# Performance work log

Measured on AMD Instinct MI355X. Metric: run time of the kernel, lower is better.

The kernel has to match this reference:

```python
import jax, jax.numpy as jnp
import numpy as np

E = 1024
H = 16
HD = 64
DI = E // 16  # 64, GRU hidden size
VOCAB = 32000
B, T = 2, 2048


def adaptive_pool_matrix(l_in, l_out):
    # PyTorch AdaptiveAvgPool1d: out[i] = mean(in[floor(i*l_in/l_out) : ceil((i+1)*l_in/l_out)])
    P = np.zeros((l_in, l_out), np.float32)
    for i in range(l_out):
        s = (i * l_in) // l_out
        e = -((-(i + 1) * l_in) // l_out)
        P[s:e, i] = 1.0 / (e - s)
    return jnp.asarray(P)


def gru(x, wih, whh):
    # x: [B, T, DI]; wih/whh: [3*DI, DI]; no bias; gate order (r, z, n)
    h_dim = whh.shape[1]
    xw = jnp.einsum('btd,gd->btg', x, wih)  # [B, T, 3*DI]

    def step(h, xw_t):
        hw = h @ whh.T
        r = jax.nn.sigmoid(xw_t[:, :h_dim] + hw[:, :h_dim])
        z = jax.nn.sigmoid(xw_t[:, h_dim:2 * h_dim] + hw[:, h_dim:2 * h_dim])
        n = jnp.tanh(xw_t[:, 2 * h_dim:] + r * hw[:, 2 * h_dim:])
        h_new = (1.0 - z) * n + z * h
        return h_new, h_new

    h0 = jnp.zeros((x.shape[0], h_dim), x.dtype)
    _, hs = jax.lax.scan(step, h0, jnp.swapaxes(xw, 0, 1))
    return jnp.swapaxes(hs, 0, 1)  # [B, T, DI]


def pos_embed(x, gru_wih, gru_whh, lin_w, p_pos, p_proj):
    # x: [B, T, E]. Pools act on the feature dim (torch last-dim after permute).
    x_proj = x @ p_proj            # [B, T, E-DI]
    pos = gru(x @ p_pos, gru_wih, gru_whh)  # [B, T, DI]
    out = jnp.concatenate([pos, x_proj], axis=-1) @ lin_w.T
    return out + x


def layernorm(x, w, b, eps=1e-5):
    mu = jnp.mean(x, axis=-1, keepdims=True)
    var = jnp.var(x, axis=-1, keepdims=True)
    return (x - mu) * jax.lax.rsqrt(var + eps) * w + b


def setup_inputs() -> dict:
    key = jax.random.key(0)
    ks = jax.random.split(key, 16)
    s = 0.02
    return {
        'x': jax.random.normal(ks[0], (B, T, E), jnp.float32),
        'token_ids': jax.random.randint(ks[1], (B, T), 0, VOCAB, jnp.int32),
        'q_gru_wih': jax.random.normal(ks[2], (3 * DI, DI), jnp.float32) * s,
        'q_gru_whh': jax.random.normal(ks[3], (3 * DI, DI), jnp.float32) * s,
        'q_lin_w': jax.random.normal(ks[4], (E, E), jnp.float32) * s,
        'k_gru_wih': jax.random.normal(ks[5], (3 * DI, DI), jnp.float32) * s,
        'k_gru_whh': jax.random.normal(ks[6], (3 * DI, DI), jnp.float32) * s,
        'k_lin_w': jax.random.normal(ks[7], (E, E), jnp.float32) * s,
        'v_emb': jax.random.normal(ks[8], (VOCAB, E), jnp.float32) * s + 1.0,
        'q_ln_w': jnp.ones((E,), jnp.float32),
        'q_ln_b': jnp.zeros((E,), jnp.float32),
        'k_ln_w': jnp.ones((E,), jnp.float32),
        'k_ln_b': jnp.zeros((E,), jnp.float32),
        'out_w': jax.random.normal(ks[9], (E, E), jnp.float32) * s,
        'out_b': jnp.zeros((E,), jnp.float32),
    }


def reference(x, token_ids, q_gru_wih, q_gru_whh, q_lin_w, k_gru_wih, k_gru_whh,
              k_lin_w, v_emb, q_ln_w, q_ln_b, k_ln_w, k_ln_b, out_w, out_b):
    p_pos = adaptive_pool_matrix(E, DI)
    p_proj = adaptive_pool_matrix(E, E - DI)

    q = pos_embed(x, q_gru_wih, q_gru_whh, q_lin_w, p_pos, p_proj)
    k = pos_embed(x, k_gru_wih, k_gru_whh, k_lin_w, p_pos, p_proj)
    v = jax.nn.silu(x) * v_emb[token_ids]  # [B, T, E]

    q = layernorm(q, q_ln_w, q_ln_b)
    k = layernorm(k, k_ln_w, k_ln_b)

    # [B, T, E] -> [B, H, T, HD]
    def split_heads(t):
        return t.reshape(B, T, H, HD).transpose(0, 2, 1, 3)

    qh, kh, vh = split_heads(q), split_heads(k), split_heads(v)

    scores = jnp.einsum('bhtd,bhsd->bhts', qh, kh) / jnp.sqrt(jnp.float32(HD))
    # Original code: attn_weights += attn_weights.masked_fill(mask, -inf)
    # => unmasked scores are DOUBLED; masked (future) positions become -inf.
    causal = jnp.triu(jnp.ones((T, T), bool), k=1)  # True above diagonal
    scores = jnp.where(causal, -jnp.inf, scores * 2.0)
    attn = jax.nn.softmax(scores, axis=-1)

    out = jnp.einsum('bhts,bhsd->bhtd', attn, vh)  # [B, H, T, HD]
    out = out.transpose(0, 2, 1, 3).reshape(B, T, E)
    return out @ out_w.T + out_b
```

## Files before the change

kernel.cpp:

```cpp
#include <hip/hip_runtime.h>


namespace {

constexpr int B_ = 2, T_ = 2048, E_ = 1024, H_ = 16, HD_ = 64, G3_ = 192, M_ = B_ * T_;
constexpr float SRg = -1.4426950408889634f;
constexpr float SNg = 2.8853900817779268f;

typedef _Float16 f16;
typedef _Float16 f16x8 __attribute__((ext_vector_type(8)));
typedef _Float16 f16x4 __attribute__((ext_vector_type(4)));
typedef _Float16 f16x2 __attribute__((ext_vector_type(2)));
typedef float f32x4 __attribute__((ext_vector_type(4)));

__device__ __forceinline__ f32x4 mfma16(f16x8 a, f16x8 b, f32x4 c) {
  return __builtin_amdgcn_mfma_f32_16x16x32_f16(a, b, c, 0, 0, 0);
}

#if __has_builtin(__builtin_amdgcn_fdot2)
__device__ __forceinline__ float fdot2(f16x2 a, f16x2 b, float c) {
  return __builtin_amdgcn_fdot2(a, b, c, false);
}
#else
__device__ __forceinline__ float fdot2(f16x2 a, f16x2 b, float c) {
  return c + (float)a[0] * (float)b[0] + (float)a[1] * (float)b[1];
}
#endif

__device__ __forceinline__ float exp2_(float x) {
#if __has_builtin(__builtin_amdgcn_exp2f)
  return __builtin_amdgcn_exp2f(x);
#else
  return exp2f(x);
#endif
}
__device__ __forceinline__ float rcp_(float x) {
#if __has_builtin(__builtin_amdgcn_rcpf)
  return __builtin_amdgcn_rcpf(x);
#else
  return 1.f / x;
#endif
}

__device__ __forceinline__ void stage_w_f32(const float* __restrict__ Wf,
                                            f16 (*Bs)[72], int n0, int kt,
                                            int tid) {
#pragma unroll
  for (int it = 0; it < 4; ++it) {
    const int r = it * 32 + (tid >> 3);
    const int cs = (tid & 7) * 8;
    const float* src = Wf + (size_t)(n0 + r) * E_ + kt + cs;
    float4 w0 = *(const float4*)src;
    float4 w1 = *(const float4*)(src + 4);
    f16x8 o = {(f16)w0.x, (f16)w0.y, (f16)w0.z, (f16)w0.w,
               (f16)w1.x, (f16)w1.y, (f16)w1.z, (f16)w1.w};
    *(f16x8*)&Bs[r][cs] = o;
  }
}

__global__ __launch_bounds__(256) void k_prep(
    const float* __restrict__ x, const int* __restrict__ tok,
    const float* __restrict__ wihq, const float* __restrict__ wihk,
    const float* __restrict__ v_emb,
    f16* __restrict__ vh, f16* __restrict__ aq, f16* __restrict__ ak,
    float* __restrict__ xwq, float* __restrict__ xwk) {
  __shared__ float xs[E_];
  __shared__ float xp[64];
  const int row = blockIdx.x;
  const int b = row >> 11, t = row & (T_ - 1);
  const int tid = threadIdx.x;
  const float* xrow = x + (size_t)row * E_;
  {
    const int tk = tok[row];
    float4 xv = ((const float4*)xrow)[tid];
    ((float4*)xs)[tid] = xv;
    float4 ev = ((const float4*)(v_emb + (size_t)tk * E_))[tid];
    f16x4 o;
    o[0] = (f16)(xv.x / (1.f + __expf(-xv.x)) * ev.x);
    o[1] = (f16)(xv.y / (1.f + __expf(-xv.y)) * ev.y);
    o[2] = (f16)(xv.z / (1.f + __expf(-xv.z)) * ev.z);
    o[3] = (f16)(xv.w / (1.f + __expf(-xv.w)) * ev.w);
    const int e0 = tid * 4;
    const size_t voff = ((size_t)(b * H_ + (e0 >> 6)) * T_ + t) * HD_ + (e0 & 63);
    *(f16x4*)(vh + voff) = o;
  }
  __syncthreads();
  if (tid < 64) {
    float s = 0.f;
#pragma unroll
    for (int j = 0; j < 16; ++j) s += xs[tid * 16 + j];
    xp[tid] = s * (1.f / 16.f);
  }
  for (int i = tid; i < 960; i += 256) {
    int s0 = (i * 1024) / 960;
    int e0 = ((i + 1) * 1024 + 959) / 960;
    float m = xs[s0];
    if (e0 - s0 == 2) m = (m + xs[s0 + 1]) * 0.5f;
    f16 hv = (f16)m;
    aq[(size_t)row * E_ + 64 + i] = hv;
    ak[(size_t)row * E_ + 64 + i] = hv;
  }
  __syncthreads();
  for (int o = tid; o < 2 * G3_; o += 256) {
    const int chain = o / G3_, g = o % G3_;
    const float* wrow = (chain ? wihk : wihq) + (size_t)g * 64;
    float acc = 0.f;
#pragma unroll
    for (int c = 0; c < 16; ++c) {
      float4 wv = *(const float4*)(wrow + c * 4);
      acc += xp[c * 4] * wv.x + xp[c * 4 + 1] * wv.y +
             xp[c * 4 + 2] * wv.z + xp[c * 4 + 3] * wv.w;
    }
    const float sc = (g < 128) ? SRg : SNg;
    (chain ? xwk : xwq)[(size_t)row * G3_ + g] = acc * sc;
  }
}

__device__ __forceinline__ void gru_core(const float* __restrict__ xw,
                                         const float* __restrict__ whh,
                                         f16* __restrict__ a, int lane) {
  __builtin_amdgcn_s_setprio(3);
  f16x2 wr[32], wz[32], wn[32];
#pragma unroll
  for (int i = 0; i < 32; ++i) {
    wr[i] = {(f16)(whh[(size_t)lane * 64 + i] * SRg),
             (f16)(whh[(size_t)lane * 64 + i + 32] * SRg)};
    wz[i] = {(f16)(whh[(size_t)(64 + lane) * 64 + i] * SRg),
             (f16)(whh[(size_t)(64 + lane) * 64 + i + 32] * SRg)};
    wn[i] = {(f16)(whh[(size_t)(128 + lane) * 64 + i] * SNg),
             (f16)(whh[(size_t)(128 + lane) * 64 + i + 32] * SNg)};
  }
  float h = 0.f;
  float xr = xw[lane], xz = xw[64 + lane], xn = xw[128 + lane];
  f16* ap = a + lane;
  for (int t = 0; t < T_; ++t) {
    const unsigned hu = (unsigned)__builtin_bit_cast(unsigned short, (f16)h);
    int va = (int)hu, vb = (int)hu;
    asm volatile("v_permlane32_swap_b32 %0, %1" : "+v"(va), "+v"(vb));
    const int pk = (int)(hu | ((unsigned)va << 16));
    const int tn = (t + 1 < T_) ? t + 1 : t;
    const float* nx = xw + (size_t)tn * G3_;
    const float nxr = nx[lane], nxz = nx[64 + lane], nxn = nx[128 + lane];
    float ar = xr, az = xz, an = 0.f;
#pragma unroll
    for (int i = 0; i < 32; ++i) {
      const f16x2 hh = __builtin_bit_cast(f16x2, __builtin_amdgcn_readlane(pk, i));
      ar = fdot2(wr[i], hh, ar);
      an = fdot2(wn[i], hh, an);
      az = fdot2(wz[i], hh, az);
    }
    const float r = rcp_(1.f + exp2_(ar));
    const float p2 = fmaf(r, an, xn);
    const float n = fmaf(-2.f, rcp_(1.f + exp2_(p2)), 1.f);
    const float z = rcp_(1.f + exp2_(az));
    h = fmaf(z, h - n, n);
    ap[(size_t)t * E_] = (f16)h;
    xr = nxr; xz = nxz; xn = nxn;
  }
}

__global__ __launch_bounds__(256, 1) void k_mega(
    const float* __restrict__ xwq, const float* __restrict__ xwk,
    const float* __restrict__ whhq, const float* __restrict__ whhk,
    f16* __restrict__ aq, f16* __restrict__ ak,
    const float* __restrict__ WQf, const float* __restrict__ WKf,
    const float* __restrict__ x,
    float* __restrict__ QPRE, float* __restrict__ KPRE,
    const float* __restrict__ out_w, f16* __restrict__ WO) {
  __shared__ __align__(16) f16 As[128][72];
  __shared__ __align__(16) f16 Bs[128][72];
  const int bx = blockIdx.x;
  const int tid = threadIdx.x;
  if (bx == 0) {
    const int wid = tid >> 6, lane = tid & 63;
    const int qk = wid >> 1, b = wid & 1;
    const float* xw = (qk ? xwk : xwq) + (size_t)b * T_ * G3_;
    const float* whh = qk ? whhk : whhq;
    f16* a = (qk ? ak : aq) + (size_t)b * T_ * E_;
    gru_core(xw, whh, a, lane);
    return;
  }
  if (bx <= 512) {
    const int bid = bx - 1;
    const int chain = bid >> 8, tile = bid & 255;
    const int m0 = (tile >> 3) * 128, n0 = (tile & 7) * 128;
    const f16* A = chain ? ak : aq;
    const float* Wf = chain ? WKf : WQf;
    float* C = chain ? KPRE : QPRE;
    const int wid = tid >> 6, lane = tid & 63;
    const int wr = wid >> 1, wc = wid & 1;
    const int lg = lane >> 4, lc = lane & 15;
    f32x4 acc[4][4] = {};
    for (int kt = 64; kt < E_; kt += 64) {
#pragma unroll
      for (int it = 0; it < 4; ++it) {
        const int r = it * 32 + (tid >> 3);
        const int cs = (tid & 7) * 8;
        *(f16x8*)&As[r][cs] = *(const f16x8*)(A + (size_t)(m0 + r) * E_ + kt + cs);
      }
      stage_w_f32(Wf, Bs, n0, kt, tid);
      __syncthreads();
      f16x8 af[4][2], bf[4][2];
#pragma unroll
      for (int mi = 0; mi < 4; ++mi)
#pragma unroll
        for (int ks = 0; ks < 2; ++ks) {
          af[mi][ks] = *(const f16x8*)&As[wr * 64 + mi * 16 + lc][ks * 32 + lg * 8];
          bf[mi][ks] = *(const f16x8*)&Bs[wc * 64 + mi * 16 + lc][ks * 32 + lg * 8];
        }
#pragma unroll
      for (int mi = 0; mi < 4; ++mi)
#pragma unroll
        for (int ni = 0; ni < 4; ++ni)
#pragma unroll
          for (int ks = 0; ks < 2; ++ks)
            acc[mi][ni] = mfma16(af[mi][ks], bf[ni][ks], acc[mi][ni]);
      __syncthreads();
    }
#pragma unroll
    for (int mi = 0; mi < 4; ++mi) {
      const int r0 = m0 + wr * 64 + mi * 16 + lg * 4;
#pragma unroll
      for (int ni = 0; ni < 4; ++ni) {
        const int col = n0 + wc * 64 + ni * 16 + lc;
#pragma unroll
        for (int q = 0; q < 4; ++q) {
          const size_t idx = (size_t)(r0 + q) * E_ + col;
          C[idx] = acc[mi][ni][q] + x[idx];
        }
      }
    }
    return;
  }
  {
    const int cb = bx - 513;
    for (int i = cb * 256 + tid; i < E_ * E_ / 4; i += 8 * 256) {
      float4 v = ((const float4*)out_w)[i];
      f16x4 o = {(f16)v.x, (f16)v.y, (f16)v.z, (f16)v.w};
      *(f16x4*)(WO + (size_t)i * 4) = o;
    }
  }
}

__global__ __launch_bounds__(256) void k_fix(
    const f16* __restrict__ aq, const f16* __restrict__ ak,
    const float* __restrict__ WQf, const float* __restrict__ WKf,
    float* __restrict__ QPRE, float* __restrict__ KPRE) {
  __shared__ __align__(16) f16 As[128][72];
  __shared__ __align__(16) f16 Bs[128][72];
  const int chain = blockIdx.z;
  const f16* A = chain ? ak : aq;
  const float* Wf = chain ? WKf : WQf;
  float* C = chain ? KPRE : QPRE;
  const int m0 = blockIdx.x * 128, n0 = blockIdx.y * 128;
  const int tid = threadIdx.x;
  const int wid = tid >> 6, lane = tid & 63;
  const int wr = wid >> 1, wc = wid & 1;
  const int lg = lane >> 4, lc = lane & 15;
#pragma unroll
  for (int it = 0; it < 4; ++it) {
    const int r = it * 32 + (tid >> 3);
    const int cs = (tid & 7) * 8;
    *(f16x8*)&As[r][cs] = *(const f16x8*)(A + (size_t)(m0 + r) * E_ + cs);
  }
  stage_w_f32(Wf, Bs, n0, 0, tid);
  __syncthreads();
  f32x4 acc[4][4] = {};
  f16x8 af[4][2], bf[4][2];
#pragma unroll
  for (int mi = 0; mi < 4; ++mi)
#pragma unroll
    for (int ks = 0; ks < 2; ++ks) {
      af[mi][ks] = *(const f16x8*)&As[wr * 64 + mi * 16 + lc][ks * 32 + lg * 8];
      bf[mi][ks] = *(const f16x8*)&Bs[wc * 64 + mi * 16 + lc][ks * 32 + lg * 8];
    }
#pragma unroll
  for (int mi = 0; mi < 4; ++mi)
#pragma unroll
    for (int ni = 0; ni < 4; ++ni)
#pragma unroll
      for (int ks = 0; ks < 2; ++ks)
        acc[mi][ni] = mfma16(af[mi][ks], bf[ni][ks], acc[mi][ni]);
#pragma unroll
  for (int mi = 0; mi < 4; ++mi) {
    const int r0 = m0 + wr * 64 + mi * 16 + lg * 4;
#pragma unroll
    for (int ni = 0; ni < 4; ++ni) {
      const int col = n0 + wc * 64 + ni * 16 + lc;
#pragma unroll
      for (int q = 0; q < 4; ++q) {
        const size_t idx = (size_t)(r0 + q) * E_ + col;
        C[idx] += acc[mi][ni][q];
      }
    }
  }
}

__global__ __launch_bounds__(256) void k_ln(
    const float* __restrict__ qpre, const float* __restrict__ kpre,
    const float* __restrict__ qw, const float* __restrict__ qb,
    const float* __restrict__ kw, const float* __restrict__ kb,
    f16* __restrict__ qh, f16* __restrict__ kh) {
  const int chain = blockIdx.y;
  const float* pre = chain ? kpre : qpre;
  const float* gw = chain ? kw : qw;
  const float* gb = chain ? kb : qb;
  f16* outp = chain ? kh : qh;
  const int row = blockIdx.x;
  const int tid = threadIdx.x;
  const float4 v = ((const float4*)(pre + (size_t)row * E_))[tid];
  float s = v.x + v.y + v.z + v.w;
  float s2 = v.x * v.x + v.y * v.y + v.z * v.z + v.w * v.w;
#pragma unroll
  for (int off = 32; off; off >>= 1) {
    s += __shfl_xor(s, off);
    s2 += __shfl_xor(s2, off);
  }
  __shared__ float red[8];
  const int wid = tid >> 6, lane = tid & 63;
  if (!lane) { red[wid] = s; red[4 + wid] = s2; }
  __syncthreads();
  s = red[0] + red[1] + red[2] + red[3];
  s2 = red[4] + red[5] + red[6] + red[7];
  const float mu = s * (1.f / E_);
  const float inv = rsqrtf(s2 * (1.f / E_) - mu * mu + 1e-5f);
  const float4 w4 = ((const float4*)gw)[tid];
  const float4 b4 = ((const float4*)gb)[tid];
  const int e0 = tid * 4;
  f16x4 o;
  o[0] = (f16)((v.x - mu) * inv * w4.x + b4.x);
  o[1] = (f16)((v.y - mu) * inv * w4.y + b4.y);
  o[2] = (f16)((v.z - mu) * inv * w4.z + b4.z);
  o[3] = (f16)((v.w - mu) * inv * w4.w + b4.w);
  const int b = row >> 11, t = row & (T_ - 1);
  const size_t off2 = ((size_t)(b * H_ + (e0 >> 6)) * T_ + t) * HD_ + (e0 & 63);
  *(f16x4*)(outp + off2) = o;
}

__global__ __launch_bounds__(256) void k_attn(const f16* __restrict__ Q,
                                              const f16* __restrict__ K,
                                              const f16* __restrict__ V,
                                              f16* __restrict__ AO) {
  __shared__ __align__(16) f16 Kt[64][72];
  __shared__ __align__(16) f16 Vt[64][72];
  __shared__ __align__(16) f16 Ps[4][16][72];
  const int qi = blockIdx.x, bh = blockIdx.y;
  const int b = bh >> 4, h = bh & 15;
  const int tid = threadIdx.x, wid = tid >> 6, lane = tid & 63;
  const int lg = lane >> 4, lc = lane & 15;
  const size_t hbase = (size_t)bh * T_ * HD_;
  const int qb = qi * 64;
  f16x8 qf[2];
  {
    const int qrow = qb + wid * 16 + lc;
#pragma unroll
    for (int ks = 0; ks < 2; ++ks)
      qf[ks] = *(const f16x8*)(Q + hbase + (size_t)qrow * HD_ + ks * 32 + lg * 8);
  }
  f32x4 o[4] = {};
  float m_run[4] = {-1e30f, -1e30f, -1e30f, -1e30f};
  float l_run[4] = {};
  const int qrow_d = qb + wid * 16 + lg * 4;
  for (int kt = 0; kt <= qi; ++kt) {
    {
      const int r = tid >> 2, cs = (tid & 3) * 16;
      const f16* ksrc = K + hbase + (size_t)(kt * 64 + r) * HD_ + cs;
      *(f16x8*)&Kt[r][cs] = *(const f16x8*)ksrc;
      *(f16x8*)&Kt[r][cs + 8] = *(const f16x8*)(ksrc + 8);
      const f16* vsrc = V + hbase + (size_t)(kt * 64 + lane) * HD_ + wid * 16;
      f16x8 va = *(const f16x8*)vsrc;
      f16x8 vb = *(const f16x8*)(vsrc + 8);
#pragma unroll
      for (int u = 0; u < 8; ++u) {
        Vt[wid * 16 + u][lane] = va[u];
        Vt[wid * 16 + 8 + u][lane] = vb[u];
      }
    }
    __syncthreads();
    f32x4 s[4] = {};
#pragma unroll
    for (int nt = 0; nt < 4; ++nt)
#pragma unroll
      for (int ks = 0; ks < 2; ++ks) {
        f16x8 kf = *(const f16x8*)&Kt[nt * 16 + lc][ks * 32 + lg * 8];
        s[nt] = mfma16(qf[ks], kf, s[nt]);
      }
    const bool diag = (kt == qi);
#pragma unroll
    for (int nt = 0; nt < 4; ++nt) {
      const int colg = kt * 64 + nt * 16 + lc;
#pragma unroll
      for (int r = 0; r < 4; ++r) {
        float v = s[nt][r] * 0.25f;
        if (diag && colg > qrow_d + r) v = -1e30f;
        s[nt][r] = v;
      }
    }
    float scalev[4];
#pragma unroll
    for (int r = 0; r < 4; ++r) {
      float m = fmaxf(fmaxf(s[0][r], s[1][r]), fmaxf(s[2][r], s[3][r]));
#pragma unroll
      for (int of = 1; of < 16; of <<= 1) m = fmaxf(m, __shfl_xor(m, of));
      const float mn = fmaxf(m_run[r], m);
      scalev[r] = __expf(m_run[r] - mn);
      m_run[r] = mn;
    }
    float ladd[4] = {};
#pragma unroll
    for (int nt = 0; nt < 4; ++nt)
#pragma unroll
      for (int r = 0; r < 4; ++r) {
        const float p = __expf(s[nt][r] - m_run[r]);
        s[nt][r] = p;
        ladd[r] += p;
      }
#pragma unroll
    for (int r = 0; r < 4; ++r) {
      float la = ladd[r];
#pragma unroll
      for (int of = 1; of < 16; of <<= 1) la += __shfl_xor(la, of);
      l_run[r] = l_run[r] * scalev[r] + la;
      o[0][r] *= scalev[r];
      o[1][r] *= scalev[r];
      o[2][r] *= scalev[r];
      o[3][r] *= scalev[r];
    }
#pragma unroll
    for (int nt = 0; nt < 4; ++nt)
#pragma unroll
      for (int r = 0; r < 4; ++r)
        Ps[wid][lg * 4 + r][nt * 16 + lc] = (f16)s[nt][r];
    f16x8 pf[2];
#pragma unroll
    for (int ks = 0; ks < 2; ++ks)
      pf[ks] = *(const f16x8*)&Ps[wid][lc][ks * 32 + lg * 8];
#pragma unroll
    for (int nt = 0; nt < 4; ++nt)
#pragma unroll
      for (int ks = 0; ks < 2; ++ks) {
        f16x8 vf = *(const f16x8*)&Vt[nt * 16 + lc][ks * 32 + lg * 8];
        o[nt] = mfma16(pf[ks], vf, o[nt]);
      }
    __syncthreads();
  }
#pragma unroll
  for (int nt = 0; nt < 4; ++nt)
#pragma unroll
    for (int r = 0; r < 4; ++r) {
      const float val = o[nt][r] / l_run[r];
      const int qrow = qrow_d + r;
      AO[((size_t)(b * T_ + qrow)) * E_ + h * HD_ + nt * 16 + lc] = (f16)val;
    }
}

__global__ __launch_bounds__(256) void k_gemm_out(
    const f16* __restrict__ A, const f16* __restrict__ W,
    const float* __restrict__ bias, float* __restrict__ C) {
  __shared__ __align__(16) f16 As[128][72];
  __shared__ __align__(16) f16 Bs[128][72];
  const int m0 = blockIdx.x * 128, n0 = blockIdx.y * 128;
  const int tid = threadIdx.x;
  const int wid = tid >> 6, lane = tid & 63;
  const int wr = wid >> 1, wc = wid & 1;
  const int lg = lane >> 4, lc = lane & 15;
  f32x4 acc[4][4] = {};
  for (int kt = 0; kt < E_; kt += 64) {
#pragma unroll
    for (int it = 0; it < 4; ++it) {
      const int r = it * 32 + (tid >> 3);
      const int cs = (tid & 7) * 8;
      *(f16x8*)&As[r][cs] = *(const f16x8*)(A + (size_t)(m0 + r) * E_ + kt + cs);
      *(f16x8*)&Bs[r][cs] = *(const f16x8*)(W + (size_t)(n0 + r) * E_ + kt + cs);
    }
    __syncthreads();
    f16x8 af[4][2], bf[4][2];
#pragma unroll
    for (int mi = 0; mi < 4; ++mi)
#pragma unroll
      for (int ks = 0; ks < 2; ++ks) {
        af[mi][ks] = *(const f16x8*)&As[wr * 64 + mi * 16 + lc][ks * 32 + lg * 8];
        bf[mi][ks] = *(const f16x8*)&Bs[wc * 64 + mi * 16 + lc][ks * 32 + lg * 8];
      }
#pragma unroll
    for (int mi = 0; mi < 4; ++mi)
#pragma unroll
      for (int ni = 0; ni < 4; ++ni)
#pragma unroll
        for (int ks = 0; ks < 2; ++ks)
          acc[mi][ni] = mfma16(af[mi][ks], bf[ni][ks], acc[mi][ni]);
    __syncthreads();
  }
#pragma unroll
  for (int mi = 0; mi < 4; ++mi) {
    const int r0 = m0 + wr * 64 + mi * 16 + lg * 4;
#pragma unroll
    for (int ni = 0; ni < 4; ++ni) {
      const int col = n0 + wc * 64 + ni * 16 + lc;
      const float bv = bias[col];
#pragma unroll
      for (int q = 0; q < 4; ++q)
        C[(size_t)(r0 + q) * E_ + col] = acc[mi][ni][q] + bv;
    }
  }
}

}

extern "C" void kernel_launch(void* const* d_in, const int* in_sizes, int n_in,
                              void* d_out, int out_size, void* d_ws, size_t ws_size,
                              hipStream_t stream) {
  (void)in_sizes; (void)n_in; (void)out_size; (void)ws_size;
  const float* x      = (const float*)d_in[0];
  const int*   tok    = (const int*)d_in[1];
  const float* q_wih  = (const float*)d_in[2];
  const float* q_whh  = (const float*)d_in[3];
  const float* q_lin  = (const float*)d_in[4];
  const float* k_wih  = (const float*)d_in[5];
  const float* k_whh  = (const float*)d_in[6];
  const float* k_lin  = (const float*)d_in[7];
  const float* v_emb  = (const float*)d_in[8];
  const float* q_ln_w = (const float*)d_in[9];
  const float* q_ln_b = (const float*)d_in[10];
  const float* k_ln_w = (const float*)d_in[11];
  const float* k_ln_b = (const float*)d_in[12];
  const float* out_w  = (const float*)d_in[13];
  const float* out_b  = (const float*)d_in[14];
  float* outp = (float*)d_out;

  char* ws = (char*)d_ws;
  size_t off = 0;
  auto take = [&](size_t bytes) -> void* {
    void* p = ws + off;
    off += (bytes + 255) & ~(size_t)255;
    return p;
  };
  f16* WO   = (f16*)take((size_t)E_ * E_ * 2);
  f16* AQ   = (f16*)take((size_t)M_ * E_ * 2);
  f16* AK   = (f16*)take((size_t)M_ * E_ * 2);
  f16* VH   = (f16*)take((size_t)M_ * E_ * 2);
  f16* QH   = (f16*)take((size_t)M_ * E_ * 2);
  f16* KH   = (f16*)take((size_t)M_ * E_ * 2);
  f16* AO   = (f16*)take((size_t)M_ * E_ * 2);
  float* XWQ  = (float*)take((size_t)M_ * G3_ * 4);
  float* XWK  = (float*)take((size_t)M_ * G3_ * 4);
  float* QPRE = (float*)take((size_t)M_ * E_ * 4);
  float* KPRE = (float*)take((size_t)M_ * E_ * 4);

  k_prep<<<dim3(M_), dim3(256), 0, stream>>>(x, tok, q_wih, k_wih, v_emb, VH, AQ, AK, XWQ, XWK);

  k_mega<<<dim3(521), dim3(256), 0, stream>>>(XWQ, XWK, q_whh, k_whh, AQ, AK,
                                              q_lin, k_lin, x, QPRE, KPRE, out_w, WO);

  k_fix<<<dim3(M_ / 128, E_ / 128, 2), dim3(256), 0, stream>>>(AQ, AK, q_lin, k_lin, QPRE, KPRE);
  k_ln<<<dim3(M_, 2), dim3(256), 0, stream>>>(QPRE, KPRE, q_ln_w, q_ln_b, k_ln_w, k_ln_b, QH, KH);

  k_attn<<<dim3(T_ / 64, B_ * H_), dim3(256), 0, stream>>>(QH, KH, VH, AO);
  k_gemm_out<<<dim3(M_ / 128, E_ / 128), dim3(256), 0, stream>>>(AO, WO, out_b, outp);
}
```

Measured before the change: 879.9 us.

## Compute GRU recurrent matvec with MFMA and LDS-broadcast hidden state

Replaces the per-step GRU hidden-state matvec with MFMA instructions. The old version used 96 fdot2 ops over readlane-broadcast packed halves plus a permlane swap. The new version writes h to a per-wave LDS buffer and reads it back as MFMA A fragments, with the scaled W_hh held as f16 B fragments in registers. Each lane then selects its gate output from the accumulator tiles. The aim is to shorten the serial per-timestep latency of the recurrence, at the cost of an LDS round trip and MFMA latency on the critical path every step.

Result: slower. 1.037 ms (+17.8%).

```diff
diff --git a/kernel.cpp b/kernel.cpp
--- a/kernel.cpp
+++ b/kernel.cpp
@@ -16,16 +16,6 @@
 __device__ __forceinline__ f32x4 mfma16(f16x8 a, f16x8 b, f32x4 c) {
   return __builtin_amdgcn_mfma_f32_16x16x32_f16(a, b, c, 0, 0, 0);
 }
-
-#if __has_builtin(__builtin_amdgcn_fdot2)
-__device__ __forceinline__ float fdot2(f16x2 a, f16x2 b, float c) {
-  return __builtin_amdgcn_fdot2(a, b, c, false);
-}
-#else
-__device__ __forceinline__ float fdot2(f16x2 a, f16x2 b, float c) {
-  return c + (float)a[0] * (float)b[0] + (float)a[1] * (float)b[1];
-}
-#endif
 
 __device__ __forceinline__ float exp2_(float x) {
 #if __has_builtin(__builtin_amdgcn_exp2f)
@@ -116,45 +106,77 @@
   }
 }
 
-__device__ __forceinline__ void gru_core(const float* __restrict__ xw,
+__device__ __forceinline__ void gru_mfma(const float* __restrict__ xw,
                                          const float* __restrict__ whh,
-                                         f16* __restrict__ a, int lane) {
+                                         f16* __restrict__ a, int lane,
+                                         f16* __restrict__ hbuf) {
   __builtin_amdgcn_s_setprio(3);
-  f16x2 wr[32], wz[32], wn[32];
-#pragma unroll
-  for (int i = 0; i < 32; ++i) {
-    wr[i] = {(f16)(whh[(size_t)lane * 64 + i] * SRg),
-             (f16)(whh[(size_t)lane * 64 + i + 32] * SRg)};
-    wz[i] = {(f16)(whh[(size_t)(64 + lane) * 64 + i] * SRg),
-             (f16)(whh[(size_t)(64 + lane) * 64 + i + 32] * SRg)};
-    wn[i] = {(f16)(whh[(size_t)(128 + lane) * 64 + i] * SNg),
-             (f16)(whh[(size_t)(128 + lane) * 64 + i + 32] * SNg)};
+  const int lc = lane & 15, lg = lane >> 4;
+  f16x8 bf[12][2];
+#pragma unroll
+  for (int t = 0; t < 12; ++t) {
+    const int g = 16 * t + lc;
+    const float sc = (g < 128) ? SRg : SNg;
+#pragma unroll
+    for (int ks = 0; ks < 2; ++ks) {
+      const float* wrow = whh + (size_t)g * 64 + 32 * ks + lg * 8;
+      float4 w0 = *(const float4*)wrow;
+      float4 w1 = *(const float4*)(wrow + 4);
+      f16x8 o = {(f16)(w0.x * sc), (f16)(w0.y * sc), (f16)(w0.z * sc), (f16)(w0.w * sc),
+                 (f16)(w1.x * sc), (f16)(w1.y * sc), (f16)(w1.z * sc), (f16)(w1.w * sc)};
+      bf[t][ks] = o;
+    }
   }
   float h = 0.f;
+  hbuf[lane] = (f16)0.f;
+  const f16* afp0 = hbuf + lg * 8;
+  const f16* afp1 = hbuf + 32 + lg * 8;
   float xr = xw[lane], xz = xw[64 + lane], xn = xw[128 + lane];
   f16* ap = a + lane;
+  const f32x4 zero4 = {0.f, 0.f, 0.f, 0.f};
   for (int t = 0; t < T_; ++t) {
-    const unsigned hu = (unsigned)__builtin_bit_cast(unsigned short, (f16)h);
-    int va = (int)hu, vb = (int)hu;
-    asm volatile("v_permlane32_swap_b32 %0, %1" : "+v"(va), "+v"(vb));
-    const int pk = (int)(hu | ((unsigned)va << 16));
+    const f16x8 a0 = *(const f16x8*)afp0;
+    const f16x8 a1 = *(const f16x8*)afp1;
     const int tn = (t + 1 < T_) ? t + 1 : t;
     const float* nx = xw + (size_t)tn * G3_;
     const float nxr = nx[lane], nxz = nx[64 + lane], nxn = nx[128 + lane];
-    float ar = xr, az = xz, an = 0.f;
-#pragma unroll
-    for (int i = 0; i < 32; ++i) {
-      const f16x2 hh = __builtin_bit_cast(f16x2, __builtin_amdgcn_readlane(pk, i));
-      ar = fdot2(wr[i], hh, ar);
-      an = fdot2(wn[i], hh, an);
-      az = fdot2(wz[i], hh, az);
-    }
+    f32x4 acc0 = mfma16(a0, bf[0][0], zero4);
+    f32x4 acc1 = mfma16(a0, bf[1][0], zero4);
+    f32x4 acc2 = mfma16(a0, bf[2][0], zero4);
+    f32x4 acc3 = mfma16(a0, bf[3][0], zero4);
+    f32x4 acc4 = mfma16(a0, bf[4][0], zero4);
+    f32x4 acc5 = mfma16(a0, bf[5][0], zero4);
+    f32x4 acc6 = mfma16(a0, bf[6][0], zero4);
+    f32x4 acc7 = mfma16(a0, bf[7][0], zero4);
+    f32x4 acc8 = mfma16(a0, bf[8][0], zero4);
+    f32x4 acc9 = mfma16(a0, bf[9][0], zero4);
+    f32x4 acc10 = mfma16(a0, bf[10][0], zero4);
+    f32x4 acc11 = mfma16(a0, bf[11][0], zero4);
+    acc0 = mfma16(a1, bf[0][1], acc0);
+    acc1 = mfma16(a1, bf[1][1], acc1);
+    acc2 = mfma16(a1, bf[2][1], acc2);
+    acc3 = mfma16(a1, bf[3][1], acc3);
+    acc4 = mfma16(a1, bf[4][1], acc4);
+    acc5 = mfma16(a1, bf[5][1], acc5);
+    acc6 = mfma16(a1, bf[6][1], acc6);
+    acc7 = mfma16(a1, bf[7][1], acc7);
+    acc8 = mfma16(a1, bf[8][1], acc8);
+    acc9 = mfma16(a1, bf[9][1], acc9);
+    acc10 = mfma16(a1, bf[10][1], acc10);
+    acc11 = mfma16(a1, bf[11][1], acc11);
+    const float arv = (lg == 0) ? acc0[0] : (lg == 1) ? acc1[0] : (lg == 2) ? acc2[0] : acc3[0];
+    const float azv = (lg == 0) ? acc4[0] : (lg == 1) ? acc5[0] : (lg == 2) ? acc6[0] : acc7[0];
+    const float anv = (lg == 0) ? acc8[0] : (lg == 1) ? acc9[0] : (lg == 2) ? acc10[0] : acc11[0];
+    const float ar = xr + arv;
+    const float az = xz + azv;
     const float r = rcp_(1.f + exp2_(ar));
-    const float p2 = fmaf(r, an, xn);
+    const float p2 = fmaf(r, anv, xn);
     const float n = fmaf(-2.f, rcp_(1.f + exp2_(p2)), 1.f);
     const float z = rcp_(1.f + exp2_(az));
     h = fmaf(z, h - n, n);
-    ap[(size_t)t * E_] = (f16)h;
+    const f16 h16 = (f16)h;
+    ap[(size_t)t * E_] = h16;
+    hbuf[lane] = h16;
     xr = nxr; xz = nxz; xn = nxn;
   }
 }
@@ -174,10 +196,11 @@
   if (bx == 0) {
     const int wid = tid >> 6, lane = tid & 63;
     const int qk = wid >> 1, b = wid & 1;
-    const float* xw = (qk ? xwk : xwq) + (size_t)b * T_ * G3_;
+    const float* xw = ((qk ? xwk : xwq)) + (size_t)b * T_ * G3_;
     const float* whh = qk ? whhk : whhq;
     f16* a = (qk ? ak : aq) + (size_t)b * T_ * E_;
-    gru_core(xw, whh, a, lane);
+    f16* hbuf = &As[0][0] + wid * 64;
+    gru_mfma(xw, whh, a, lane, hbuf);
     return;
   }
   if (bx <= 512) {
```
